# Performance work log

Measured on AMD Instinct MI355X. Metric: run time of the kernel, lower is better.

Reference implementation:

```python
import jax, jax.numpy as jnp
import numpy as np

N = 200000
E = 5000000


def _gcn_norm(edge_index, num_nodes):
    # add self-loops and compute symmetric normalization (PyG GCNConv default)
    loop = jnp.arange(num_nodes, dtype=edge_index.dtype)
    src = jnp.concatenate([edge_index[0], loop])
    dst = jnp.concatenate([edge_index[1], loop])
    ones = jnp.ones(dst.shape[0], dtype=jnp.float32)
    deg = jax.ops.segment_sum(ones, dst, num_segments=num_nodes)
    dis = jnp.where(deg > 0, jax.lax.rsqrt(deg), 0.0)
    norm = dis[src] * dis[dst]  # [E+N]
    return src, dst, norm


def _gcn_layer(x, src, dst, norm, W, b, num_nodes):
    xl = x @ W  # [N, out] dense linear (no bias, PyG default)
    msg = xl[src] * norm[:, None]  # gather + scale
    agg = jax.ops.segment_sum(msg, dst, num_segments=num_nodes)  # scatter-add
    return agg + b


def setup_inputs() -> dict:
    key = jax.random.key(0)
    ks = jax.random.split(key, 10)
    x = jax.random.normal(ks[0], (N, 12), dtype=jnp.float32)
    edge_index = jax.random.randint(ks[1], (2, E), 0, N, dtype=jnp.int64)
    def glorot(k, fi, fo):
        s = np.sqrt(6.0 / (fi + fo)).astype(np.float32)
        return jax.random.uniform(k, (fi, fo), jnp.float32, -s, s)
    return {
        "x": x,
        "edge_index": edge_index,
        "W1": glorot(ks[2], 12, 16), "b1": jnp.zeros((16,), jnp.float32),
        "W2": glorot(ks[3], 16, 8), "b2": jnp.zeros((8,), jnp.float32),
        "W3": glorot(ks[4], 8, 16), "b3": jnp.zeros((16,), jnp.float32),
        "W4": glorot(ks[5], 16, 12), "b4": jnp.zeros((12,), jnp.float32),
    }


def reference(x, edge_index, W1, b1, W2, b2, W3, b3, W4, b4):
    num_nodes = x.shape[0]
    src, dst, norm = _gcn_norm(edge_index, num_nodes)
    # Encoder
    h = jax.nn.relu(_gcn_layer(x, src, dst, norm, W1, b1, num_nodes))
    h = _gcn_layer(h, src, dst, norm, W2, b2, num_nodes)
    # Decoder
    h = jax.nn.relu(_gcn_layer(h, src, dst, norm, W3, b3, num_nodes))
    h = jax.nn.sigmoid(_gcn_layer(h, src, dst, norm, W4, b4, num_nodes))
    return h
```

## Files before the change

### kernel.cpp

```cpp
#include <hip/hip_runtime.h>
#include <hip/hip_fp16.h>
#include <math.h>


#define NPB 1024
#define MAX_NB 256
#define CAP 26496
#define BIN_CHUNK 4096
#define BIN_TH 512
#define EPT (BIN_CHUNK / BIN_TH)
#define MAXB CAP

__global__ void init_cur_kernel(int* __restrict__ bucket_cur, int NB) {
    int t = blockIdx.x * blockDim.x + threadIdx.x;
    if (t < NB) bucket_cur[t] = t * CAP;
}

__global__ __launch_bounds__(BIN_TH) void bin_kernel(const int* __restrict__ src,
                                                     const int* __restrict__ dst,
                                                     int* __restrict__ bucket_cur,
                                                     unsigned int* __restrict__ binned,
                                                     int E, int NB) {
    __shared__ int h[MAX_NB];
    __shared__ int scl[MAX_NB + 1];
    __shared__ int base[MAX_NB];
    __shared__ int sscan[256];
    __shared__ unsigned int stage[BIN_CHUNK];
    __shared__ unsigned char bkt8[BIN_CHUNK];
    int cbeg = blockIdx.x * BIN_CHUNK;
    int cend = min(cbeg + BIN_CHUNK, E);
    int chunk_n = cend - cbeg;
    int tid = threadIdx.x;

    for (int t = tid; t < NB; t += BIN_TH) h[t] = 0;
    __syncthreads();
    int myd[EPT];
#pragma unroll
    for (int j = 0; j < EPT; j++) {
        int e = cbeg + tid + j * BIN_TH;
        if (e < cend) {
            myd[j] = dst[e];
            atomicAdd(&h[myd[j] >> 10], 1);
        }
    }
    __syncthreads();
    int v = (tid < NB) ? h[tid] : 0;
    if (tid < 256) sscan[tid] = v;
    __syncthreads();
    for (int off = 1; off < 256; off <<= 1) {
        int t = (tid >= off && tid < 256) ? sscan[tid - off] : 0;
        __syncthreads();
        if (tid < 256) sscan[tid] += t;
        __syncthreads();
    }
    if (tid < NB) {
        scl[tid] = sscan[tid] - v;
        base[tid] = v ? atomicAdd(&bucket_cur[tid], v) : 0;
    }
    if (tid == 0) scl[NB] = chunk_n;
    __syncthreads();
    for (int t = tid; t < NB; t += BIN_TH) h[t] = 0;
    __syncthreads();
#pragma unroll
    for (int j = 0; j < EPT; j++) {
        int e = cbeg + tid + j * BIN_TH;
        if (e < cend) {
            int d = myd[j];
            int bkt = d >> 10;
            int pos = scl[bkt] + atomicAdd(&h[bkt], 1);
            stage[pos] = ((unsigned)src[e] << 10) | (unsigned)(d & 1023);
            bkt8[pos] = (unsigned char)bkt;
        }
    }
    __syncthreads();
    for (int k = tid; k < chunk_n; k += BIN_TH) {
        int bkt = bkt8[k];
        binned[base[bkt] + (k - scl[bkt])] = stage[k];
    }
}

__global__ __launch_bounds__(1024) void csr_bucket_t1_kernel(
    const unsigned int* __restrict__ binned,
    const int* __restrict__ bucket_cur,
    int2* __restrict__ rows, float* __restrict__ dis,
    int* __restrict__ col,
    const float* __restrict__ x,
    __half* __restrict__ xls, int N) {
    __shared__ int cnt[NPB];
    __shared__ int cur[NPB];
    __shared__ int colbuf[MAXB];
    int b = blockIdx.x;
    int nbase = b << 10;
    int nlocal = min(NPB, N - nbase);
    int beg = b * CAP;
    int bsize = bucket_cur[b] - beg;
    int tid = threadIdx.x;

    cnt[tid] = 0;
    __syncthreads();
    for (int k = tid; k < bsize; k += 1024)
        atomicAdd(&cnt[binned[beg + k] & 1023u], 1);
    __syncthreads();
    int v = cnt[tid];
    cur[tid] = v;
    __syncthreads();
    for (int off = 1; off < 1024; off <<= 1) {
        int t = (tid >= off) ? cur[tid - off] : 0;
        __syncthreads();
        cur[tid] += t;
        __syncthreads();
    }
    int excl = cur[tid] - v;
    float d = 1.0f / sqrtf((float)(v + 1));
    if (tid < nlocal) {
        rows[nbase + tid] = make_int2(beg + excl, beg + excl + v);
        dis[nbase + tid] = d;
    }
    __syncthreads();
    cur[tid] = excl;
    __syncthreads();
    if (bsize <= MAXB) {
        for (int k = tid; k < bsize; k += 1024) {
            unsigned rec = binned[beg + k];
            int pos = atomicAdd(&cur[rec & 1023u], 1);
            colbuf[pos] = (int)(rec >> 10);
        }
        __syncthreads();
        for (int k = tid; k < bsize; k += 1024) col[beg + k] = colbuf[k];
    } else {
        for (int k = tid; k < bsize; k += 1024) {
            unsigned rec = binned[beg + k];
            int pos = atomicAdd(&cur[rec & 1023u], 1);
            col[beg + pos] = (int)(rec >> 10);
        }
    }
    if (tid < nlocal) {
        int i = nbase + tid;
        float h[12];
#pragma unroll
        for (int k = 0; k < 12; k++) h[k] = x[(size_t)i * 12 + k];
        __half2* x2 = (__half2*)xls;
#pragma unroll
        for (int c = 0; c < 2; c++) {
#pragma unroll
            for (int k = 0; k < 3; k++) {
                x2[(size_t)c * N * 3 + (size_t)i * 3 + k] =
                    __floats2half2_rn(h[6 * c + 2 * k] * d, h[6 * c + 2 * k + 1] * d);
            }
        }
    }
}

template <int P>
__device__ __forceinline__ void acc_node(const __half2* __restrict__ x2, int c,
                                         float2 (&acc)[P]) {
    __half2 t[P];
#pragma unroll
    for (int k = 0; k < P; k++) t[k] = x2[(size_t)c * P + k];
#pragma unroll
    for (int k = 0; k < P; k++) {
        float2 v = __half22float2(t[k]);
        acc[k].x += v.x;
        acc[k].y += v.y;
    }
}

template <int P>
__device__ __forceinline__ void acc_quad(const __half2* __restrict__ x2, int4 c,
                                         float2 (&acc)[P]) {
    __half2 t[4][P];
#pragma unroll
    for (int k = 0; k < P; k++) t[0][k] = x2[(size_t)c.x * P + k];
#pragma unroll
    for (int k = 0; k < P; k++) t[1][k] = x2[(size_t)c.y * P + k];
#pragma unroll
    for (int k = 0; k < P; k++) t[2][k] = x2[(size_t)c.z * P + k];
#pragma unroll
    for (int k = 0; k < P; k++) t[3][k] = x2[(size_t)c.w * P + k];
#pragma unroll
    for (int k = 0; k < P; k++) {
        float2 a0 = __half22float2(t[0][k]), a1 = __half22float2(t[1][k]);
        float2 a2 = __half22float2(t[2][k]), a3 = __half22float2(t[3][k]);
        acc[k].x += (a0.x + a1.x) + (a2.x + a3.x);
        acc[k].y += (a0.y + a1.y) + (a2.y + a3.y);
    }
}

template <int C>
__device__ __forceinline__ void gather_acc(
    int i, int p, const int2* __restrict__ rows, const int* __restrict__ col,
    const __half2* __restrict__ x2, float2 (&acc)[C / 2]) {
    constexpr int P = C / 2;
#pragma unroll
    for (int k = 0; k < P; k++) {
        if (p == 0) acc[k] = __half22float2(x2[(size_t)i * P + k]);
        else acc[k] = make_float2(0.0f, 0.0f);
    }
    int2 r = rows[i];
    int beg = r.x;
    int end = r.y;
    int nedge = end - beg;
    int pre = (4 - (beg & 3)) & 3;
    if (pre > nedge) pre = nedge;
    for (int j = p; j < pre; j += 2) acc_node<P>(x2, col[beg + j], acc);
    int abeg = beg + pre;
    int nq = (end - abeg) >> 2;
    int q = p;
    for (; q + 4 < nq; q += 6) {
        int4 ca = *reinterpret_cast<const int4*>(col + abeg + 4 * q);
        int4 cb = *reinterpret_cast<const int4*>(col + abeg + 4 * (q + 2));
        int4 cc = *reinterpret_cast<const int4*>(col + abeg + 4 * (q + 4));
        acc_quad<P>(x2, ca, acc);
        acc_quad<P>(x2, cb, acc);
        acc_quad<P>(x2, cc, acc);
    }
    for (; q < nq; q += 2) {
        int4 ca = *reinterpret_cast<const int4*>(col + abeg + 4 * q);
        acc_quad<P>(x2, ca, acc);
    }
    int tbeg = abeg + 4 * nq;
    for (int j = tbeg + p; j < end; j += 2) acc_node<P>(x2, col[j], acc);
#pragma unroll
    for (int k = 0; k < P; k++) {
        acc[k].x += __shfl_xor(acc[k].x, 1);
        acc[k].y += __shfl_xor(acc[k].y, 1);
    }
}

template <int C>
__global__ __launch_bounds__(256) void gather2_kernel(
    const int2* __restrict__ rows, const int* __restrict__ col,
    const float* __restrict__ dis, const __half* __restrict__ x0,
    const __half* __restrict__ x1, float* __restrict__ agg0,
    float* __restrict__ agg1, int N) {
    constexpr int P = C / 2;
    int grp = blockIdx.x >> 3;
    int sub = blockIdx.x & 7;
    int chunk = sub >> 2;
    int range = (grp << 2) + (sub & 3);
    int t2 = range * 256 + (int)threadIdx.x;
    int i = t2 >> 1;
    int p = t2 & 1;
    if (i >= N) return;
    const __half2* x2 = (const __half2*)(chunk ? x1 : x0);
    float* aggc = chunk ? agg1 : agg0;
    float2 acc[P];
    gather_acc<C>(i, p, rows, col, x2, acc);
    float d = dis[i];
    float2* ap = (float2*)(aggc + (size_t)i * C);
#pragma unroll
    for (int k = 0; k < P; k++) {
        if ((k & 1) == p) ap[k] = make_float2(acc[k].x * d, acc[k].y * d);
    }
}

__global__ __launch_bounds__(256) void transform12_kernel(
    const float* __restrict__ a0, const float* __restrict__ a1,
    const float* __restrict__ b1, const float* __restrict__ W1,
    const float* __restrict__ W2, const float* __restrict__ dis,
    __half* __restrict__ xout, int N) {
    __shared__ float sW1[12 * 16];
    __shared__ float sW2[16 * 8];
    __shared__ float sB[16];
    if (threadIdx.x < 192) sW1[threadIdx.x] = W1[threadIdx.x];
    if (threadIdx.x < 128) sW2[threadIdx.x] = W2[threadIdx.x];
    if (threadIdx.x < 16) sB[threadIdx.x] = b1[threadIdx.x];
    __syncthreads();
    int i = blockIdx.x * blockDim.x + threadIdx.x;
    if (i >= N) return;
    float A[12];
#pragma unroll
    for (int k = 0; k < 6; k++) {
        A[k] = a0[(size_t)i * 6 + k];
        A[6 + k] = a1[(size_t)i * 6 + k];
    }
    float h[16];
#pragma unroll
    for (int f = 0; f < 16; f++) {
        float acc = sB[f];
#pragma unroll
        for (int k = 0; k < 12; k++) acc = fmaf(A[k], sW1[k * 16 + f], acc);
        h[f] = fmaxf(acc, 0.0f);
    }
    float d = dis[i];
    __half2* x2 = (__half2*)xout;
#pragma unroll
    for (int k2 = 0; k2 < 4; k2++) {
        float o0 = 0.0f, o1 = 0.0f;
#pragma unroll
        for (int k = 0; k < 16; k++) {
            o0 = fmaf(h[k], sW2[k * 8 + 2 * k2], o0);
            o1 = fmaf(h[k], sW2[k * 8 + 2 * k2 + 1], o1);
        }
        x2[(size_t)i * 4 + k2] = __floats2half2_rn(o0 * d, o1 * d);
    }
}

__global__ __launch_bounds__(256) void gather8_t3_kernel(
    const int2* __restrict__ rows, const int* __restrict__ col,
    const float* __restrict__ dis, const __half* __restrict__ xin,
    const float* __restrict__ b2, __half* __restrict__ xout, int N) {
    int tid = blockIdx.x * blockDim.x + threadIdx.x;
    int i = tid >> 1;
    int p = tid & 1;
    if (i >= N) return;
    float2 acc[4];
    gather_acc<8>(i, p, rows, col, (const __half2*)xin, acc);
    float d = dis[i];
    __half2* x2o = (__half2*)xout;
#pragma unroll
    for (int k = 0; k < 4; k++) {
        if ((k >> 1) == p) {
            x2o[(size_t)i * 4 + k] =
                __floats2half2_rn((acc[k].x * d + b2[2 * k]) * d,
                                  (acc[k].y * d + b2[2 * k + 1]) * d);
        }
    }
}

__global__ __launch_bounds__(256) void gather8_t4_kernel(
    const int2* __restrict__ rows, const int* __restrict__ col,
    const float* __restrict__ dis, const __half* __restrict__ xin,
    const float* __restrict__ b3, const float* __restrict__ W3,
    const float* __restrict__ W4, __half* __restrict__ xout, int N) {
    __shared__ float sW3[8 * 16];
    __shared__ float sW4[16 * 12];
    __shared__ float sB[16];
    if (threadIdx.x < 128) sW3[threadIdx.x] = W3[threadIdx.x];
    if (threadIdx.x < 192) sW4[threadIdx.x] = W4[threadIdx.x];
    if (threadIdx.x < 16) sB[threadIdx.x] = b3[threadIdx.x];
    __syncthreads();
    int tid = blockIdx.x * blockDim.x + threadIdx.x;
    int i = tid >> 1;
    int p = tid & 1;
    if (i >= N) return;
    float2 acc[4];
    gather_acc<8>(i, p, rows, col, (const __half2*)xin, acc);
    float d = dis[i];
    float A[8];
#pragma unroll
    for (int k = 0; k < 4; k++) {
        A[2 * k] = acc[k].x * d;
        A[2 * k + 1] = acc[k].y * d;
    }
    float h[8];
#pragma unroll
    for (int f = 0; f < 8; f++) {
        float a = sB[p * 8 + f];
#pragma unroll
        for (int k = 0; k < 8; k++) a = fmaf(A[k], sW3[k * 16 + p * 8 + f], a);
        h[f] = fmaxf(a, 0.0f);
    }
    float o[12];
#pragma unroll
    for (int j = 0; j < 12; j++) {
        float a = 0.0f;
#pragma unroll
        for (int f = 0; f < 8; f++) a = fmaf(h[f], sW4[(p * 8 + f) * 12 + j], a);
        o[j] = a;
    }
#pragma unroll
    for (int j = 0; j < 12; j++) o[j] += __shfl_xor(o[j], 1);
    __half2* x2o = (__half2*)xout;
#pragma unroll
    for (int k = 0; k < 3; k++) {
        x2o[(size_t)p * N * 3 + (size_t)i * 3 + k] =
            __floats2half2_rn(o[6 * p + 2 * k] * d, o[6 * p + 2 * k + 1] * d);
    }
}

__global__ __launch_bounds__(256) void gather2_sig_kernel(
    const int2* __restrict__ rows, const int* __restrict__ col,
    const float* __restrict__ dis, const __half* __restrict__ x0,
    const __half* __restrict__ x1, const float* __restrict__ bias,
    float* __restrict__ out, int N) {
    int grp = blockIdx.x >> 3;
    int sub = blockIdx.x & 7;
    int chunk = sub >> 2;
    int range = (grp << 2) + (sub & 3);
    int t2 = range * 256 + (int)threadIdx.x;
    int i = t2 >> 1;
    int p = t2 & 1;
    if (i >= N) return;
    const __half2* x2 = (const __half2*)(chunk ? x1 : x0);
    int coff = chunk ? 6 : 0;
    float2 acc[3];
    gather_acc<6>(i, p, rows, col, x2, acc);
    float d = dis[i];
    float* op = out + (size_t)i * 12 + coff;
#pragma unroll
    for (int k = 0; k < 3; k++) {
        if ((k & 1) == p) {
            float vx = 1.0f / (1.0f + expf(-(acc[k].x * d + bias[coff + 2 * k])));
            float vy = 1.0f / (1.0f + expf(-(acc[k].y * d + bias[coff + 2 * k + 1])));
            *reinterpret_cast<float2*>(op + 2 * k) = make_float2(vx, vy);
        }
    }
}

static inline size_t align_up(size_t v, size_t a) { return (v + a - 1) & ~(a - 1); }

extern "C" void kernel_launch(void* const* d_in, const int* in_sizes, int n_in,
                              void* d_out, int out_size, void* d_ws, size_t ws_size,
                              hipStream_t stream) {
    const float* x  = (const float*)d_in[0];
    const int*   ei = (const int*)d_in[1];
    const float* W1 = (const float*)d_in[2];
    const float* b1 = (const float*)d_in[3];
    const float* W2 = (const float*)d_in[4];
    const float* b2 = (const float*)d_in[5];
    const float* W3 = (const float*)d_in[6];
    const float* b3 = (const float*)d_in[7];
    const float* W4 = (const float*)d_in[8];
    const float* b4 = (const float*)d_in[9];
    float* out = (float*)d_out;

    const int N = in_sizes[0] / 12;
    const int E = in_sizes[1] / 2;
    const int* src = ei;
    const int* dst = ei + E;
    const int NB = (N + NPB - 1) / NPB;

    char* ws = (char*)d_ws;
    size_t off = 0;
    int* bucket_cur = (int*)(ws + off);   off = align_up(off + (size_t)NB * 4, 256);
    int2* rows = (int2*)(ws + off);       off = align_up(off + (size_t)N * 8, 256);
    float* dis = (float*)(ws + off);      off = align_up(off + (size_t)N * 4, 256);
    unsigned int* binned = (unsigned int*)(ws + off);
    off = align_up(off + ((size_t)NB * CAP + 4096) * 4, 256);
    int* col = (int*)(ws + off);          off = align_up(off + ((size_t)NB * CAP + 4096) * 4, 256);
    __half* xls = (__half*)(ws + off);    off = align_up(off + (size_t)N * 16 * 2, 256);
    __half* xls2 = (__half*)(ws + off);   off = align_up(off + (size_t)N * 16 * 2, 256);
    float* aggA = (float*)(ws + off);     off = align_up(off + (size_t)N * 16 * 4, 256);
    (void)ws_size; (void)n_in; (void)out_size;

    const int B = 256;
    auto blocks = [&](long long n) { return (int)((n + B - 1) / B); };
    int nb2 = blocks(2LL * N);
    nb2 = (nb2 + 3) & ~3;
    const int G2 = nb2 * 2;

    init_cur_kernel<<<1, 256, 0, stream>>>(bucket_cur, NB);
    bin_kernel<<<(E + BIN_CHUNK - 1) / BIN_CHUNK, BIN_TH, 0, stream>>>(src, dst, bucket_cur, binned, E, NB);
    csr_bucket_t1_kernel<<<NB, 1024, 0, stream>>>(binned, bucket_cur, rows, dis, col,
                                                  x, xls, N);

    __half* x_c0 = xls;
    __half* x_c6 = xls + (size_t)N * 6;
    __half* t4_c0 = xls2;
    __half* t4_c6 = xls2 + (size_t)N * 6;
    float* aggA0 = aggA;
    float* aggA1 = aggA + (size_t)N * 6;

    gather2_kernel<6><<<G2, B, 0, stream>>>(rows, col, dis, x_c0, x_c6, aggA0, aggA1, N);

    transform12_kernel<<<blocks(N), B, 0, stream>>>(aggA0, aggA1, b1, W1, W2, dis, xls2, N);

    gather8_t3_kernel<<<blocks(2LL * N), B, 0, stream>>>(rows, col, dis, xls2, b2, xls, N);

    gather8_t4_kernel<<<blocks(2LL * N), B, 0, stream>>>(rows, col, dis, xls, b3, W3, W4,
                                                         xls2, N);

    gather2_sig_kernel<<<G2, B, 0, stream>>>(rows, col, dis, t4_c0, t4_c6, b4, out, N);
}
```

Measured before the change: 358.2 us.

## Gather all 12 features per node in one pass instead of two 6-wide chunks

Switches the 12-channel feature buffers from two planar 6-wide halves to an interleaved 12-wide-per-node layout. The first and last GCN aggregations now run as single kernels that read each node's CSR row once and gather 24-byte rows, rather than two passes over the edge list with 12-byte rows each. The unroll depth of the edge loop is reduced for wide rows to limit register pressure. The trade-off is larger per-edge gathers and more registers per thread against halving the col reads and the row traversals.

```diff
diff --git a/kernel.cpp b/kernel.cpp
--- a/kernel.cpp
+++ b/kernel.cpp
@@ -141,12 +141,9 @@
         for (int k = 0; k < 12; k++) h[k] = x[(size_t)i * 12 + k];
         __half2* x2 = (__half2*)xls;
 #pragma unroll
-        for (int c = 0; c < 2; c++) {
-#pragma unroll
-            for (int k = 0; k < 3; k++) {
-                x2[(size_t)c * N * 3 + (size_t)i * 3 + k] =
-                    __floats2half2_rn(h[6 * c + 2 * k] * d, h[6 * c + 2 * k + 1] * d);
-            }
+        for (int k = 0; k < 6; k++) {
+            x2[(size_t)i * 6 + k] =
+                __floats2half2_rn(h[2 * k] * d, h[2 * k + 1] * d);
         }
     }
 }
@@ -191,6 +188,7 @@
     int i, int p, const int2* __restrict__ rows, const int* __restrict__ col,
     const __half2* __restrict__ x2, float2 (&acc)[C / 2]) {
     constexpr int P = C / 2;
+    constexpr int UN = (P >= 6) ? 2 : 3;
 #pragma unroll
     for (int k = 0; k < P; k++) {
         if (p == 0) acc[k] = __half22float2(x2[(size_t)i * P + k]);
@@ -206,13 +204,13 @@
     int abeg = beg + pre;
     int nq = (end - abeg) >> 2;
     int q = p;
-    for (; q + 4 < nq; q += 6) {
-        int4 ca = *reinterpret_cast<const int4*>(col + abeg + 4 * q);
-        int4 cb = *reinterpret_cast<const int4*>(col + abeg + 4 * (q + 2));
-        int4 cc = *reinterpret_cast<const int4*>(col + abeg + 4 * (q + 4));
-        acc_quad<P>(x2, ca, acc);
-        acc_quad<P>(x2, cb, acc);
-        acc_quad<P>(x2, cc, acc);
+    for (; q + 2 * (UN - 1) < nq; q += 2 * UN) {
+        int4 cs[UN];
+#pragma unroll
+        for (int u = 0; u < UN; u++)
+            cs[u] = *reinterpret_cast<const int4*>(col + abeg + 4 * (q + 2 * u));
+#pragma unroll
+        for (int u = 0; u < UN; u++) acc_quad<P>(x2, cs[u], acc);
     }
     for (; q < nq; q += 2) {
         int4 ca = *reinterpret_cast<const int4*>(col + abeg + 4 * q);
@@ -227,35 +225,26 @@
     }
 }
 
-template <int C>
-__global__ __launch_bounds__(256) void gather2_kernel(
+__global__ __launch_bounds__(256) void gather12_kernel(
     const int2* __restrict__ rows, const int* __restrict__ col,
-    const float* __restrict__ dis, const __half* __restrict__ x0,
-    const __half* __restrict__ x1, float* __restrict__ agg0,
-    float* __restrict__ agg1, int N) {
-    constexpr int P = C / 2;
-    int grp = blockIdx.x >> 3;
-    int sub = blockIdx.x & 7;
-    int chunk = sub >> 2;
-    int range = (grp << 2) + (sub & 3);
-    int t2 = range * 256 + (int)threadIdx.x;
-    int i = t2 >> 1;
-    int p = t2 & 1;
+    const float* __restrict__ dis, const __half* __restrict__ xin,
+    float* __restrict__ agg, int N) {
+    int tid = blockIdx.x * blockDim.x + threadIdx.x;
+    int i = tid >> 1;
+    int p = tid & 1;
     if (i >= N) return;
-    const __half2* x2 = (const __half2*)(chunk ? x1 : x0);
-    float* aggc = chunk ? agg1 : agg0;
-    float2 acc[P];
-    gather_acc<C>(i, p, rows, col, x2, acc);
+    float2 acc[6];
+    gather_acc<12>(i, p, rows, col, (const __half2*)xin, acc);
     float d = dis[i];
-    float2* ap = (float2*)(aggc + (size_t)i * C);
-#pragma unroll
-    for (int k = 0; k < P; k++) {
+    float2* ap = (float2*)(agg + (size_t)i * 12);
+#pragma unroll
+    for (int k = 0; k < 6; k++) {
         if ((k & 1) == p) ap[k] = make_float2(acc[k].x * d, acc[k].y * d);
     }
 }
 
 __global__ __launch_bounds__(256) void transform12_kernel(
-    const float* __restrict__ a0, const float* __restrict__ a1,
+    const float* __restrict__ a0,
     const float* __restrict__ b1, const float* __restrict__ W1,
     const float* __restrict__ W2, const float* __restrict__ dis,
     __half* __restrict__ xout, int N) {
@@ -270,10 +259,7 @@
     if (i >= N) return;
     float A[12];
 #pragma unroll
-    for (int k = 0; k < 6; k++) {
-        A[k] = a0[(size_t)i * 6 + k];
-        A[6 + k] = a1[(size_t)i * 6 + k];
-    }
+    for (int k = 0; k < 12; k++) A[k] = a0[(size_t)i * 12 + k];
     float h[16];
 #pragma unroll
     for (int f = 0; f < 16; f++) {
@@ -364,35 +350,28 @@
     __half2* x2o = (__half2*)xout;
 #pragma unroll
     for (int k = 0; k < 3; k++) {
-        x2o[(size_t)p * N * 3 + (size_t)i * 3 + k] =
+        x2o[(size_t)i * 6 + p * 3 + k] =
             __floats2half2_rn(o[6 * p + 2 * k] * d, o[6 * p + 2 * k + 1] * d);
     }
 }
 
-__global__ __launch_bounds__(256) void gather2_sig_kernel(
+__global__ __launch_bounds__(256) void gather12_sig_kernel(
     const int2* __restrict__ rows, const int* __restrict__ col,
-    const float* __restrict__ dis, const __half* __restrict__ x0,
-    const __half* __restrict__ x1, const float* __restrict__ bias,
-    float* __restrict__ out, int N) {
-    int grp = blockIdx.x >> 3;
-    int sub = blockIdx.x & 7;
-    int chunk = sub >> 2;
-    int range = (grp << 2) + (sub & 3);
-    int t2 = range * 256 + (int)threadIdx.x;
-    int i = t2 >> 1;
-    int p = t2 & 1;
+    const float* __restrict__ dis, const __half* __restrict__ xin,
+    const float* __restrict__ bias, float* __restrict__ out, int N) {
+    int tid = blockIdx.x * blockDim.x + threadIdx.x;
+    int i = tid >> 1;
+    int p = tid & 1;
     if (i >= N) return;
-    const __half2* x2 = (const __half2*)(chunk ? x1 : x0);
-    int coff = chunk ? 6 : 0;
-    float2 acc[3];
-    gather_acc<6>(i, p, rows, col, x2, acc);
+    float2 acc[6];
+    gather_acc<12>(i, p, rows, col, (const __half2*)xin, acc);
     float d = dis[i];
-    float* op = out + (size_t)i * 12 + coff;
-#pragma unroll
-    for (int k = 0; k < 3; k++) {
+    float* op = out + (size_t)i * 12;
+#pragma unroll
+    for (int k = 0; k < 6; k++) {
         if ((k & 1) == p) {
-            float vx = 1.0f / (1.0f + expf(-(acc[k].x * d + bias[coff + 2 * k])));
-            float vy = 1.0f / (1.0f + expf(-(acc[k].y * d + bias[coff + 2 * k + 1])));
+            float vx = 1.0f / (1.0f + expf(-(acc[k].x * d + bias[2 * k])));
+            float vy = 1.0f / (1.0f + expf(-(acc[k].y * d + bias[2 * k + 1])));
             *reinterpret_cast<float2*>(op + 2 * k) = make_float2(vx, vy);
         }
     }
@@ -431,35 +410,25 @@
     int* col = (int*)(ws + off);          off = align_up(off + ((size_t)NB * CAP + 4096) * 4, 256);
     __half* xls = (__half*)(ws + off);    off = align_up(off + (size_t)N * 16 * 2, 256);
     __half* xls2 = (__half*)(ws + off);   off = align_up(off + (size_t)N * 16 * 2, 256);
-    float* aggA = (float*)(ws + off);     off = align_up(off + (size_t)N * 16 * 4, 256);
+    float* aggA = (float*)(ws + off);     off = align_up(off + (size_t)N * 12 * 4, 256);
     (void)ws_size; (void)n_in; (void)out_size;
 
     const int B = 256;
     auto blocks = [&](long long n) { return (int)((n + B - 1) / B); };
-    int nb2 = blocks(2LL * N);
-    nb2 = (nb2 + 3) & ~3;
-    const int G2 = nb2 * 2;
 
     init_cur_kernel<<<1, 256, 0, stream>>>(bucket_cur, NB);
     bin_kernel<<<(E + BIN_CHUNK - 1) / BIN_CHUNK, BIN_TH, 0, stream>>>(src, dst, bucket_cur, binned, E, NB);
     csr_bucket_t1_kernel<<<NB, 1024, 0, stream>>>(binned, bucket_cur, rows, dis, col,
                                                   x, xls, N);
 
-    __half* x_c0 = xls;
-    __half* x_c6 = xls + (size_t)N * 6;
-    __half* t4_c0 = xls2;
-    __half* t4_c6 = xls2 + (size_t)N * 6;
-    float* aggA0 = aggA;
-    float* aggA1 = aggA + (size_t)N * 6;
-
-    gather2_kernel<6><<<G2, B, 0, stream>>>(rows, col, dis, x_c0, x_c6, aggA0, aggA1, N);
-
-    transform12_kernel<<<blocks(N), B, 0, stream>>>(aggA0, aggA1, b1, W1, W2, dis, xls2, N);
+    gather12_kernel<<<blocks(2LL * N), B, 0, stream>>>(rows, col, dis, xls, aggA, N);
+
+    transform12_kernel<<<blocks(N), B, 0, stream>>>(aggA, b1, W1, W2, dis, xls2, N);
 
     gather8_t3_kernel<<<blocks(2LL * N), B, 0, stream>>>(rows, col, dis, xls2, b2, xls, N);
 
     gather8_t4_kernel<<<blocks(2LL * N), B, 0, stream>>>(rows, col, dis, xls, b3, W3, W4,
                                                          xls2, N);
 
-    gather2_sig_kernel<<<G2, B, 0, stream>>>(rows, col, dis, t4_c0, t4_c6, b4, out, N);
-}
+    gather12_sig_kernel<<<blocks(2LL * N), B, 0, stream>>>(rows, col, dis, xls2, b4, out, N);
+}
```

Result: slower. 371.7 us (+3.8%).
